# Kernel optimization log

Hardware: AMD Instinct MI355X
Metric: run time of the kernel (lower is better)

Reference implementation:

```python
import jax, jax.numpy as jnp
import numpy as np

HIDDEN = 2048
NUM_HEADS = 16
HEAD_DIM = HIDDEN // NUM_HEADS  # 128
LAYER_IDX = 0


def setup_inputs() -> dict:
    key = jax.random.key(0)
    k1, k2, k3, k4, k5 = jax.random.split(key, 5)
    B, S = 2, 2048
    hidden_states = jax.random.normal(k1, (B, S, HIDDEN), dtype=jnp.float32)
    # causal mask, broadcastable to attn shape (B, Q, H, K)
    causal = jnp.tril(jnp.ones((S, S), dtype=jnp.bool_))  # [Q, K]
    attention_mask = causal[None, :, None, :]  # [1, Q, 1, K]
    c_attn_w = jax.random.normal(k2, (HIDDEN, HIDDEN + 2 * HEAD_DIM), dtype=jnp.float32) * 0.02
    c_attn_b = jax.random.normal(k3, (HIDDEN + 2 * HEAD_DIM,), dtype=jnp.float32) * 0.02
    c_proj_w = jax.random.normal(k4, (HIDDEN, HIDDEN), dtype=jnp.float32) * 0.02
    c_proj_b = jax.random.normal(k5, (HIDDEN,), dtype=jnp.float32) * 0.02
    return {
        "hidden_states": hidden_states,
        "attention_mask": attention_mask,
        "c_attn_w": c_attn_w,
        "c_attn_b": c_attn_b,
        "c_proj_w": c_proj_w,
        "c_proj_b": c_proj_b,
    }


def reference(hidden_states, attention_mask, c_attn_w, c_attn_b, c_proj_w, c_proj_b):
    B, S, D = hidden_states.shape
    H, hd = NUM_HEADS, HEAD_DIM
    # c_attn then split into per-head query and shared (MQA) key/value
    qkv = hidden_states @ c_attn_w + c_attn_b  # [B, S, D + 2*hd]
    query = qkv[..., :D].reshape(B, S, H, hd)  # [B, Q, H, hd]
    k = qkv[..., D:D + hd]                     # [B, K, hd] shared across heads
    v = qkv[..., D + hd:]                      # [B, K, hd]
    # fp32 input => upcast=False => unscale=1, scale = 1/sqrt(head_dim)
    scale = 1.0 / jnp.sqrt(jnp.float32(hd))
    scores = jnp.einsum('bqhd,bkd->bqhk', query, k) * scale  # [B, Q, H, K]
    mask_value = jnp.finfo(jnp.float32).min
    scores = jnp.where(attention_mask, scores, mask_value)
    attn = jax.nn.softmax(scores, axis=-1)
    attn_output = jnp.einsum('bqhk,bkd->bqhd', attn, v).reshape(B, S, D)
    attn_output = attn_output @ c_proj_w + c_proj_b
    return attn_output
```

## Files before the change

### kernel.cpp

```cpp
#include <hip/hip_runtime.h>
#include <hip/hip_bf16.h>

typedef __bf16 bf16_t;
typedef __bf16 bf16x8 __attribute__((ext_vector_type(8)));
typedef __bf16 bf16x4 __attribute__((ext_vector_type(4)));
typedef float f32x4 __attribute__((ext_vector_type(4)));

#define S_LEN 2048
#define HID   2048
#define NH    16
#define HD    128
#define QKVN  2304
#define NEG_BIG (-30000.0f)

__device__ __forceinline__ void gld_lds16(const bf16_t* g, bf16_t* l) {
  __builtin_amdgcn_global_load_lds(
      (const __attribute__((address_space(1))) void*)((const void*)g),
      (__attribute__((address_space(3))) void*)((void*)l), 16, 0, 0);
}

__global__ __launch_bounds__(256) void cvt_f32_bf16_kernel(
    const float* __restrict__ in, bf16_t* __restrict__ out, int n)
{
  int i = (blockIdx.x * 256 + threadIdx.x) * 4;
  if (i < n) {
    float4 v = *(const float4*)(in + i);
    bf16x4 o;
    o[0] = (bf16_t)v.x; o[1] = (bf16_t)v.y; o[2] = (bf16_t)v.z; o[3] = (bf16_t)v.w;
    *(bf16x4*)(out + i) = o;
  }
}

__global__ __launch_bounds__(256) void transpose_cvt_kernel(
    const float* __restrict__ in, bf16_t* __restrict__ out, int K, int N)
{
  int nc = threadIdx.x & 63;
  int kg = threadIdx.x >> 6;
  int n  = blockIdx.x * 64 + nc;
  int kb = blockIdx.y * 32 + kg * 8;
  bf16x8 v;
  #pragma unroll
  for (int i = 0; i < 8; ++i) v[i] = (bf16_t)in[(size_t)(kb + i) * N + n];
  *(bf16x8*)(out + (size_t)n * K + kb) = v;
}

__global__ __launch_bounds__(256) void vt_extract_kernel(
    const bf16_t* __restrict__ qkv, bf16_t* __restrict__ vtg)
{
  int d  = threadIdx.x & 127;
  int sg = threadIdx.x >> 7;
  int b  = blockIdx.y;
  int s8 = blockIdx.x * 2 + sg;
  bf16x8 v;
  #pragma unroll
  for (int i = 0; i < 8; ++i)
    v[i] = qkv[((size_t)(b * S_LEN + s8 * 8 + i)) * QKVN + HID + HD + d];
  *(bf16x8*)(vtg + ((size_t)(b * HD + d)) * S_LEN + s8 * 8) = v;
}

template <typename OutT>
__global__ __launch_bounds__(256) void gemm_bias_kernel(
    const bf16_t* __restrict__ A, const bf16_t* __restrict__ WT,
    const float* __restrict__ bias, OutT* __restrict__ C,
    int K, int lda, int ldc)
{
  __shared__ bf16_t Ash[128 * 64];
  __shared__ bf16_t Bsh[128 * 64];

  const int tid  = threadIdx.x;
  const int wave = tid >> 6;
  const int lane = tid & 63;
  const int quad = lane >> 4;
  const int c16  = lane & 15;
  const int wm = wave >> 1;
  const int wn = wave & 1;
  const int n0 = blockIdx.x * 128;
  const int m0 = blockIdx.y * 128;

  f32x4 acc[4][4] = {};

  for (int k0 = 0; k0 < K; k0 += 64) {
    __syncthreads();
    #pragma unroll
    for (int j = 0; j < 4; ++j) {
      int cbase = wave * 256 + j * 64;
      int c = cbase + lane;
      int row = c >> 3;
      int kcl = (c ^ row) & 7;
      gld_lds16(A  + (size_t)(m0 + row) * lda + k0 + kcl * 8, Ash + cbase * 8);
      gld_lds16(WT + (size_t)(n0 + row) * K   + k0 + kcl * 8, Bsh + cbase * 8);
    }
    __syncthreads();

    #pragma unroll
    for (int kk = 0; kk < 2; ++kk) {
      bf16x8 af[4], bfr[4];
      #pragma unroll
      for (int rb = 0; rb < 4; ++rb) {
        int row = wm * 64 + rb * 16 + c16;
        int kcp = ((kk * 4 + quad) ^ row) & 7;
        af[rb] = *(const bf16x8*)(Ash + row * 64 + kcp * 8);
      }
      #pragma unroll
      for (int nt = 0; nt < 4; ++nt) {
        int row = wn * 64 + nt * 16 + c16;
        int kcp = ((kk * 4 + quad) ^ row) & 7;
        bfr[nt] = *(const bf16x8*)(Bsh + row * 64 + kcp * 8);
      }
      #pragma unroll
      for (int rb = 0; rb < 4; ++rb)
        #pragma unroll
        for (int nt = 0; nt < 4; ++nt)
          acc[rb][nt] = __builtin_amdgcn_mfma_f32_16x16x32_bf16(af[rb], bfr[nt],
                                                                acc[rb][nt], 0, 0, 0);
    }
  }

  #pragma unroll
  for (int nt = 0; nt < 4; ++nt) {
    int col = n0 + wn * 64 + nt * 16 + c16;
    float bv = bias[col];
    #pragma unroll
    for (int rb = 0; rb < 4; ++rb) {
      int rbase = m0 + wm * 64 + rb * 16 + quad * 4;
      #pragma unroll
      for (int r = 0; r < 4; ++r)
        C[(size_t)(rbase + r) * ldc + col] = (OutT)(acc[rb][nt][r] + bv);
    }
  }
}

__global__ __launch_bounds__(512, 4) void mqa_attn_kernel(
    const bf16_t* __restrict__ qkv, const bf16_t* __restrict__ vtg,
    bf16_t* __restrict__ out)
{
  __shared__ bf16_t Ksh[2][64 * 136];
  __shared__ bf16_t VTsh[2][128 * 72];

  const int tid  = threadIdx.x;
  const int wave = tid >> 6;
  const int g    = wave >> 2;
  const int wv   = wave & 3;
  const int lane = tid & 63;
  const int quad = lane >> 4;
  const int c16  = lane & 15;
  const int gt   = tid & 255;
  const int h = blockIdx.y;
  const int b = blockIdx.z;
  const float qscale = 0.08838834764831845f * 1.4426950408889634f;

  const bf16_t* kbase = qkv + (size_t)b * S_LEN * QKVN + HID;
  const bf16_t* vtb   = vtg + (size_t)b * HD * S_LEN;

  for (int half = 0; half < 2; ++half) {
    const int qb = half ? (31 - (int)blockIdx.x) : (int)blockIdx.x;
    const int q0 = qb * 64;
    const int qrow = q0 + wv * 16 + c16;

    const bf16_t* qp = qkv + ((size_t)(b * S_LEN + qrow)) * QKVN + h * HD;
    bf16x8 qf[4];
    #pragma unroll
    for (int ks = 0; ks < 4; ++ks) {
      bf16x8 t = *(const bf16x8*)(qp + ks * 32 + quad * 8);
      #pragma unroll
      for (int j = 0; j < 8; ++j) t[j] = (bf16_t)((float)t[j] * qscale);
      qf[ks] = t;
    }

    float m_q = NEG_BIG, l_q = 0.0f;
    f32x4 o[8] = {};
    const int nss = (qb + 2) >> 1;

    for (int ss = 0; ss < nss; ++ss) {
      const int kt = 2 * ss + g;
      const bool active = (kt <= qb);

      __syncthreads();
      if (active) {
        for (int c = gt; c < 1024; c += 256) {
          int key = c >> 4, dc = c & 15;
          *(bf16x8*)(&Ksh[g][key * 136 + dc * 8]) =
              *(const bf16x8*)(kbase + (size_t)(kt * 64 + key) * QKVN + dc * 8);
        }
        for (int c = gt; c < 1024; c += 256) {
          int d = c >> 3, kc = c & 7;
          *(bf16x8*)(&VTsh[g][d * 72 + kc * 8]) =
              *(const bf16x8*)(vtb + (size_t)d * S_LEN + kt * 64 + kc * 8);
        }
      }
      __syncthreads();

      float p[4][4];
      if (active) {
        f32x4 sacc[4] = {};
        #pragma unroll
        for (int mt = 0; mt < 4; ++mt) {
          #pragma unroll
          for (int ks = 0; ks < 4; ++ks) {
            bf16x8 kf = *(const bf16x8*)(&Ksh[g][(mt * 16 + c16) * 136 + ks * 32 + quad * 8]);
            sacc[mt] = __builtin_amdgcn_mfma_f32_16x16x32_bf16(kf, qf[ks], sacc[mt], 0, 0, 0);
          }
        }
        float mx = NEG_BIG;
        if (kt == qb) {
          #pragma unroll
          for (int mt = 0; mt < 4; ++mt) {
            #pragma unroll
            for (int r = 0; r < 4; ++r) {
              int key = kt * 64 + mt * 16 + quad * 4 + r;
              float v = sacc[mt][r];
              if (key > qrow) v = NEG_BIG;
              p[mt][r] = v;
              mx = fmaxf(mx, v);
            }
          }
        } else {
          #pragma unroll
          for (int mt = 0; mt < 4; ++mt) {
            #pragma unroll
            for (int r = 0; r < 4; ++r) {
              p[mt][r] = sacc[mt][r];
              mx = fmaxf(mx, sacc[mt][r]);
            }
          }
        }
        mx = fmaxf(mx, __shfl_xor(mx, 16));
        mx = fmaxf(mx, __shfl_xor(mx, 32));

        float mn = fmaxf(m_q, mx);
        float alpha = __builtin_exp2f(m_q - mn);
        m_q = mn;

        float rs = 0.f;
        #pragma unroll
        for (int mt = 0; mt < 4; ++mt) {
          #pragma unroll
          for (int r = 0; r < 4; ++r) {
            float pe = __builtin_exp2f(p[mt][r] - m_q);
            p[mt][r] = pe;
            rs += pe;
          }
        }
        rs += __shfl_xor(rs, 16);
        rs += __shfl_xor(rs, 32);
        l_q = l_q * alpha + rs;
        #pragma unroll
        for (int mt8 = 0; mt8 < 8; ++mt8) {
          #pragma unroll
          for (int r = 0; r < 4; ++r) o[mt8][r] *= alpha;
        }
      }

      __syncthreads();
      if (active) {
        bf16_t* Pw = &Ksh[g][(wv * 16) * 136];
        #pragma unroll
        for (int mt = 0; mt < 4; ++mt) {
          bf16x4 pk;
          #pragma unroll
          for (int r = 0; r < 4; ++r) pk[r] = (bf16_t)p[mt][r];
          *(bf16x4*)(Pw + c16 * 136 + mt * 16 + quad * 4) = pk;
        }
        bf16x8 pf[2];
        #pragma unroll
        for (int kh = 0; kh < 2; ++kh)
          pf[kh] = *(const bf16x8*)(Pw + c16 * 136 + kh * 32 + quad * 8);
        #pragma unroll
        for (int mt8 = 0; mt8 < 8; ++mt8) {
          #pragma unroll
          for (int kh = 0; kh < 2; ++kh) {
            bf16x8 vf = *(const bf16x8*)(&VTsh[g][(mt8 * 16 + c16) * 72 + kh * 32 + quad * 8]);
            o[mt8] = __builtin_amdgcn_mfma_f32_16x16x32_bf16(vf, pf[kh], o[mt8], 0, 0, 0);
          }
        }
      }
    }

    __syncthreads();
    float* scr = (float*)&VTsh[0][0];
    float* mls = scr + 4 * 16 * 132;
    if (g == 1) {
      float* op = scr + (wv * 16 + c16) * 132;
      #pragma unroll
      for (int mt8 = 0; mt8 < 8; ++mt8)
        *(f32x4*)(op + mt8 * 16 + quad * 4) = o[mt8];
      if (quad == 0) {
        mls[wv * 32 + c16] = m_q;
        mls[wv * 32 + 16 + c16] = l_q;
      }
    }
    __syncthreads();
    if (g == 0) {
      float m1 = mls[wv * 32 + c16];
      float l1 = mls[wv * 32 + 16 + c16];
      float mF = fmaxf(m_q, m1);
      float a0 = __builtin_exp2f(m_q - mF);
      float a1 = __builtin_exp2f(m1 - mF);
      float inv = 1.0f / fmaxf(a0 * l_q + a1 * l1, 1e-20f);
      a0 *= inv; a1 *= inv;
      const float* op = scr + (wv * 16 + c16) * 132;
      bf16_t* Osh = &Ksh[0][(wv * 16) * 136];
      #pragma unroll
      for (int mt8 = 0; mt8 < 8; ++mt8) {
        f32x4 o1 = *(const f32x4*)(op + mt8 * 16 + quad * 4);
        bf16x4 pk;
        #pragma unroll
        for (int r = 0; r < 4; ++r) pk[r] = (bf16_t)(o[mt8][r] * a0 + o1[r] * a1);
        *(bf16x4*)(Osh + c16 * 136 + mt8 * 16 + quad * 4) = pk;
      }
      int ql = lane >> 2, dc = lane & 3;
      #pragma unroll
      for (int i = 0; i < 4; ++i) {
        bf16x8 v = *(const bf16x8*)(Osh + ql * 136 + dc * 8 + i * 32);
        *(bf16x8*)(out + ((size_t)(b * S_LEN + q0 + wv * 16 + ql)) * HID
                       + h * HD + dc * 8 + i * 32) = v;
      }
    }
  }
}

extern "C" void kernel_launch(void* const* d_in, const int* in_sizes, int n_in,
                              void* d_out, int out_size, void* d_ws, size_t ws_size,
                              hipStream_t stream) {
  const float* hidden_f   = (const float*)d_in[0];
  const float* c_attn_w_f = (const float*)d_in[2];
  const float* c_attn_b_f = (const float*)d_in[3];
  const float* c_proj_w_f = (const float*)d_in[4];
  const float* c_proj_b_f = (const float*)d_in[5];
  float* out = (float*)d_out;

  const int M = 2 * S_LEN;
  const int nH  = M * HID;
  const int nWq = HID * QKVN;
  const int nWp = HID * HID;

  bf16_t* hbf   = (bf16_t*)d_ws;
  bf16_t* wqT   = hbf  + nH;
  bf16_t* wpT   = wqT  + nWq;
  bf16_t* qkv   = wpT  + nWp;
  bf16_t* attn  = qkv  + (size_t)M * QKVN;
  bf16_t* vtg   = attn + (size_t)M * HID;

  cvt_f32_bf16_kernel<<<nH / 1024, 256, 0, stream>>>(hidden_f, hbf, nH);
  dim3 gt1(QKVN / 64, HID / 32);
  transpose_cvt_kernel<<<gt1, 256, 0, stream>>>(c_attn_w_f, wqT, HID, QKVN);
  dim3 gt2(HID / 64, HID / 32);
  transpose_cvt_kernel<<<gt2, 256, 0, stream>>>(c_proj_w_f, wpT, HID, HID);

  dim3 g1(QKVN / 128, M / 128);
  gemm_bias_kernel<bf16_t><<<g1, 256, 0, stream>>>(hbf, wqT, c_attn_b_f, qkv,
                                                   HID, HID, QKVN);

  dim3 gv(S_LEN / 16, 2);
  vt_extract_kernel<<<gv, 256, 0, stream>>>(qkv, vtg);

  dim3 g2(16, NH, 2);
  mqa_attn_kernel<<<g2, 512, 0, stream>>>(qkv, vtg, attn);

  dim3 g3(HID / 128, M / 128);
  gemm_bias_kernel<float><<<g3, 256, 0, stream>>>(attn, wpT, c_proj_b_f, out,
                                                  HID, HID, HID);
}
```

Measured before the change: 341.5 us.

## Split attention waves across query blocks and narrow GEMM tiles to 128x64

The attention kernel no longer splits keys between two wave groups and merges partial softmax states at the end. Now the two groups own different query blocks (bx and 31-bx) and share one K/V tile per step, so the cross-group merge goes away and the K/V footprint drops to a single buffer, allowing higher occupancy. The GEMM tile is narrowed to 128x64 with launch bounds of 4 blocks, doubling the grid for better CU fill at the cost of more A-tile reloads. The attention loop now runs 32-bx steps for both groups, so the group with the smaller query block sits idle for part of it.

After: 519.4 us. 1.52x slower.

```diff
diff --git a/kernel.cpp b/kernel.cpp
--- a/kernel.cpp
+++ b/kernel.cpp
@@ -59,13 +59,13 @@
 }
 
 template <typename OutT>
-__global__ __launch_bounds__(256) void gemm_bias_kernel(
+__global__ __launch_bounds__(256, 4) void gemm_bias_kernel(
     const bf16_t* __restrict__ A, const bf16_t* __restrict__ WT,
     const float* __restrict__ bias, OutT* __restrict__ C,
     int K, int lda, int ldc)
 {
   __shared__ bf16_t Ash[128 * 64];
-  __shared__ bf16_t Bsh[128 * 64];
+  __shared__ bf16_t Bsh[64 * 64];
 
   const int tid  = threadIdx.x;
   const int wave = tid >> 6;
@@ -74,10 +74,10 @@
   const int c16  = lane & 15;
   const int wm = wave >> 1;
   const int wn = wave & 1;
-  const int n0 = blockIdx.x * 128;
+  const int n0 = blockIdx.x * 64;
   const int m0 = blockIdx.y * 128;
 
-  f32x4 acc[4][4] = {};
+  f32x4 acc[4][2] = {};
 
   for (int k0 = 0; k0 < K; k0 += 64) {
     __syncthreads();
@@ -87,14 +87,21 @@
       int c = cbase + lane;
       int row = c >> 3;
       int kcl = (c ^ row) & 7;
-      gld_lds16(A  + (size_t)(m0 + row) * lda + k0 + kcl * 8, Ash + cbase * 8);
-      gld_lds16(WT + (size_t)(n0 + row) * K   + k0 + kcl * 8, Bsh + cbase * 8);
+      gld_lds16(A + (size_t)(m0 + row) * lda + k0 + kcl * 8, Ash + cbase * 8);
+    }
+    #pragma unroll
+    for (int j = 0; j < 2; ++j) {
+      int cbase = wave * 128 + j * 64;
+      int c = cbase + lane;
+      int row = c >> 3;
+      int kcl = (c ^ row) & 7;
+      gld_lds16(WT + (size_t)(n0 + row) * K + k0 + kcl * 8, Bsh + cbase * 8);
     }
     __syncthreads();
 
     #pragma unroll
     for (int kk = 0; kk < 2; ++kk) {
-      bf16x8 af[4], bfr[4];
+      bf16x8 af[4], bfr[2];
       #pragma unroll
       for (int rb = 0; rb < 4; ++rb) {
         int row = wm * 64 + rb * 16 + c16;
@@ -102,23 +109,23 @@
         af[rb] = *(const bf16x8*)(Ash + row * 64 + kcp * 8);
       }
       #pragma unroll
-      for (int nt = 0; nt < 4; ++nt) {
-        int row = wn * 64 + nt * 16 + c16;
+      for (int nt = 0; nt < 2; ++nt) {
+        int row = wn * 32 + nt * 16 + c16;
         int kcp = ((kk * 4 + quad) ^ row) & 7;
         bfr[nt] = *(const bf16x8*)(Bsh + row * 64 + kcp * 8);
       }
       #pragma unroll
       for (int rb = 0; rb < 4; ++rb)
         #pragma unroll
-        for (int nt = 0; nt < 4; ++nt)
+        for (int nt = 0; nt < 2; ++nt)
           acc[rb][nt] = __builtin_amdgcn_mfma_f32_16x16x32_bf16(af[rb], bfr[nt],
                                                                 acc[rb][nt], 0, 0, 0);
     }
   }
 
   #pragma unroll
-  for (int nt = 0; nt < 4; ++nt) {
-    int col = n0 + wn * 64 + nt * 16 + c16;
+  for (int nt = 0; nt < 2; ++nt) {
+    int col = n0 + wn * 32 + nt * 16 + c16;
     float bv = bias[col];
     #pragma unroll
     for (int rb = 0; rb < 4; ++rb) {
@@ -130,12 +137,13 @@
   }
 }
 
-__global__ __launch_bounds__(512, 4) void mqa_attn_kernel(
+__global__ __launch_bounds__(512, 8) void mqa_attn_kernel(
     const bf16_t* __restrict__ qkv, const bf16_t* __restrict__ vtg,
     bf16_t* __restrict__ out)
 {
-  __shared__ bf16_t Ksh[2][64 * 136];
-  __shared__ bf16_t VTsh[2][128 * 72];
+  __shared__ bf16_t SM[64 * 136 + 128 * 72];
+  bf16_t* Ksh  = SM;
+  bf16_t* VTsh = SM + 64 * 136;
 
   const int tid  = threadIdx.x;
   const int wave = tid >> 6;
@@ -144,178 +152,150 @@
   const int lane = tid & 63;
   const int quad = lane >> 4;
   const int c16  = lane & 15;
-  const int gt   = tid & 255;
-  const int h = blockIdx.y;
-  const int b = blockIdx.z;
+  const int bx = blockIdx.x;
+  const int h  = blockIdx.y;
+  const int b  = blockIdx.z;
   const float qscale = 0.08838834764831845f * 1.4426950408889634f;
 
   const bf16_t* kbase = qkv + (size_t)b * S_LEN * QKVN + HID;
   const bf16_t* vtb   = vtg + (size_t)b * HD * S_LEN;
 
-  for (int half = 0; half < 2; ++half) {
-    const int qb = half ? (31 - (int)blockIdx.x) : (int)blockIdx.x;
-    const int q0 = qb * 64;
-    const int qrow = q0 + wv * 16 + c16;
-
-    const bf16_t* qp = qkv + ((size_t)(b * S_LEN + qrow)) * QKVN + h * HD;
-    bf16x8 qf[4];
-    #pragma unroll
-    for (int ks = 0; ks < 4; ++ks) {
-      bf16x8 t = *(const bf16x8*)(qp + ks * 32 + quad * 8);
-      #pragma unroll
-      for (int j = 0; j < 8; ++j) t[j] = (bf16_t)((float)t[j] * qscale);
-      qf[ks] = t;
-    }
-
-    float m_q = NEG_BIG, l_q = 0.0f;
-    f32x4 o[8] = {};
-    const int nss = (qb + 2) >> 1;
-
-    for (int ss = 0; ss < nss; ++ss) {
-      const int kt = 2 * ss + g;
-      const bool active = (kt <= qb);
-
-      __syncthreads();
-      if (active) {
-        for (int c = gt; c < 1024; c += 256) {
-          int key = c >> 4, dc = c & 15;
-          *(bf16x8*)(&Ksh[g][key * 136 + dc * 8]) =
-              *(const bf16x8*)(kbase + (size_t)(kt * 64 + key) * QKVN + dc * 8);
-        }
-        for (int c = gt; c < 1024; c += 256) {
-          int d = c >> 3, kc = c & 7;
-          *(bf16x8*)(&VTsh[g][d * 72 + kc * 8]) =
-              *(const bf16x8*)(vtb + (size_t)d * S_LEN + kt * 64 + kc * 8);
-        }
-      }
-      __syncthreads();
-
-      float p[4][4];
-      if (active) {
-        f32x4 sacc[4] = {};
-        #pragma unroll
-        for (int mt = 0; mt < 4; ++mt) {
-          #pragma unroll
-          for (int ks = 0; ks < 4; ++ks) {
-            bf16x8 kf = *(const bf16x8*)(&Ksh[g][(mt * 16 + c16) * 136 + ks * 32 + quad * 8]);
-            sacc[mt] = __builtin_amdgcn_mfma_f32_16x16x32_bf16(kf, qf[ks], sacc[mt], 0, 0, 0);
-          }
-        }
-        float mx = NEG_BIG;
-        if (kt == qb) {
-          #pragma unroll
-          for (int mt = 0; mt < 4; ++mt) {
-            #pragma unroll
-            for (int r = 0; r < 4; ++r) {
-              int key = kt * 64 + mt * 16 + quad * 4 + r;
-              float v = sacc[mt][r];
-              if (key > qrow) v = NEG_BIG;
-              p[mt][r] = v;
-              mx = fmaxf(mx, v);
-            }
-          }
-        } else {
-          #pragma unroll
-          for (int mt = 0; mt < 4; ++mt) {
-            #pragma unroll
-            for (int r = 0; r < 4; ++r) {
-              p[mt][r] = sacc[mt][r];
-              mx = fmaxf(mx, sacc[mt][r]);
-            }
-          }
-        }
-        mx = fmaxf(mx, __shfl_xor(mx, 16));
-        mx = fmaxf(mx, __shfl_xor(mx, 32));
-
-        float mn = fmaxf(m_q, mx);
-        float alpha = __builtin_exp2f(m_q - mn);
-        m_q = mn;
-
-        float rs = 0.f;
+  const int qb = g ? (31 - bx) : bx;
+  const int q0 = qb * 64;
+  const int qrow = q0 + wv * 16 + c16;
+
+  const bf16_t* qp = qkv + ((size_t)(b * S_LEN + qrow)) * QKVN + h * HD;
+  bf16x8 qf[4];
+  #pragma unroll
+  for (int ks = 0; ks < 4; ++ks) {
+    bf16x8 t = *(const bf16x8*)(qp + ks * 32 + quad * 8);
+    #pragma unroll
+    for (int j = 0; j < 8; ++j) t[j] = (bf16_t)((float)t[j] * qscale);
+    qf[ks] = t;
+  }
+
+  float m_q = NEG_BIG, l_q = 0.0f;
+  f32x4 o[8] = {};
+  const int nss = 32 - bx;
+
+  for (int kt = 0; kt < nss; ++kt) {
+    const bool active = (kt <= qb);
+
+    __syncthreads();
+    for (int c = tid; c < 1024; c += 512) {
+      int key = c >> 4, dc = c & 15;
+      *(bf16x8*)(Ksh + key * 136 + dc * 8) =
+          *(const bf16x8*)(kbase + (size_t)(kt * 64 + key) * QKVN + dc * 8);
+    }
+    for (int c = tid; c < 1024; c += 512) {
+      int d = c >> 3, kc = c & 7;
+      *(bf16x8*)(VTsh + d * 72 + kc * 8) =
+          *(const bf16x8*)(vtb + (size_t)d * S_LEN + kt * 64 + kc * 8);
+    }
+    __syncthreads();
+
+    float p[4][4];
+    if (active) {
+      f32x4 sacc[4] = {};
+      #pragma unroll
+      for (int mt = 0; mt < 4; ++mt) {
+        #pragma unroll
+        for (int ks = 0; ks < 4; ++ks) {
+          bf16x8 kf = *(const bf16x8*)(Ksh + (mt * 16 + c16) * 136 + ks * 32 + quad * 8);
+          sacc[mt] = __builtin_amdgcn_mfma_f32_16x16x32_bf16(kf, qf[ks], sacc[mt], 0, 0, 0);
+        }
+      }
+      float mx = NEG_BIG;
+      if (kt == qb) {
         #pragma unroll
         for (int mt = 0; mt < 4; ++mt) {
           #pragma unroll
           for (int r = 0; r < 4; ++r) {
-            float pe = __builtin_exp2f(p[mt][r] - m_q);
-            p[mt][r] = pe;
-            rs += pe;
+            int key = kt * 64 + mt * 16 + quad * 4 + r;
+            float v = sacc[mt][r];
+            if (key > qrow) v = NEG_BIG;
+            p[mt][r] = v;
+            mx = fmaxf(mx, v);
           }
         }
-        rs += __shfl_xor(rs, 16);
-        rs += __shfl_xor(rs, 32);
-        l_q = l_q * alpha + rs;
-        #pragma unroll
-        for (int mt8 = 0; mt8 < 8; ++mt8) {
+      } else {
+        #pragma unroll
+        for (int mt = 0; mt < 4; ++mt) {
           #pragma unroll
-          for (int r = 0; r < 4; ++r) o[mt8][r] *= alpha;
-        }
-      }
-
-      __syncthreads();
-      if (active) {
-        bf16_t* Pw = &Ksh[g][(wv * 16) * 136];
-        #pragma unroll
-        for (int mt = 0; mt < 4; ++mt) {
-          bf16x4 pk;
-          #pragma unroll
-          for (int r = 0; r < 4; ++r) pk[r] = (bf16_t)p[mt][r];
-          *(bf16x4*)(Pw + c16 * 136 + mt * 16 + quad * 4) = pk;
-        }
-        bf16x8 pf[2];
-        #pragma unroll
-        for (int kh = 0; kh < 2; ++kh)
-          pf[kh] = *(const bf16x8*)(Pw + c16 * 136 + kh * 32 + quad * 8);
-        #pragma unroll
-        for (int mt8 = 0; mt8 < 8; ++mt8) {
-          #pragma unroll
-          for (int kh = 0; kh < 2; ++kh) {
-            bf16x8 vf = *(const bf16x8*)(&VTsh[g][(mt8 * 16 + c16) * 72 + kh * 32 + quad * 8]);
-            o[mt8] = __builtin_amdgcn_mfma_f32_16x16x32_bf16(vf, pf[kh], o[mt8], 0, 0, 0);
+          for (int r = 0; r < 4; ++r) {
+            p[mt][r] = sacc[mt][r];
+            mx = fmaxf(mx, sacc[mt][r]);
           }
         }
       }
-    }
-
-    __syncthreads();
-    float* scr = (float*)&VTsh[0][0];
-    float* mls = scr + 4 * 16 * 132;
-    if (g == 1) {
-      float* op = scr + (wv * 16 + c16) * 132;
-      #pragma unroll
-      for (int mt8 = 0; mt8 < 8; ++mt8)
-        *(f32x4*)(op + mt8 * 16 + quad * 4) = o[mt8];
-      if (quad == 0) {
-        mls[wv * 32 + c16] = m_q;
-        mls[wv * 32 + 16 + c16] = l_q;
-      }
-    }
-    __syncthreads();
-    if (g == 0) {
-      float m1 = mls[wv * 32 + c16];
-      float l1 = mls[wv * 32 + 16 + c16];
-      float mF = fmaxf(m_q, m1);
-      float a0 = __builtin_exp2f(m_q - mF);
-      float a1 = __builtin_exp2f(m1 - mF);
-      float inv = 1.0f / fmaxf(a0 * l_q + a1 * l1, 1e-20f);
-      a0 *= inv; a1 *= inv;
-      const float* op = scr + (wv * 16 + c16) * 132;
-      bf16_t* Osh = &Ksh[0][(wv * 16) * 136];
+      mx = fmaxf(mx, __shfl_xor(mx, 16));
+      mx = fmaxf(mx, __shfl_xor(mx, 32));
+
+      float mn = fmaxf(m_q, mx);
+      float alpha = __builtin_exp2f(m_q - mn);
+      m_q = mn;
+
+      float rs = 0.f;
+      #pragma unroll
+      for (int mt = 0; mt < 4; ++mt) {
+        #pragma unroll
+        for (int r = 0; r < 4; ++r) {
+          float pe = __builtin_exp2f(p[mt][r] - m_q);
+          p[mt][r] = pe;
+          rs += pe;
+        }
+      }
+      rs += __shfl_xor(rs, 16);
+      rs += __shfl_xor(rs, 32);
+      l_q = l_q * alpha + rs;
       #pragma unroll
       for (int mt8 = 0; mt8 < 8; ++mt8) {
-        f32x4 o1 = *(const f32x4*)(op + mt8 * 16 + quad * 4);
+        #pragma unroll
+        for (int r = 0; r < 4; ++r) o[mt8][r] *= alpha;
+      }
+    }
+
+    __syncthreads();
+    if (active) {
+      bf16_t* Pw = Ksh + (wv * 16) * 136 + g * 72;
+      #pragma unroll
+      for (int mt = 0; mt < 4; ++mt) {
         bf16x4 pk;
         #pragma unroll
-        for (int r = 0; r < 4; ++r) pk[r] = (bf16_t)(o[mt8][r] * a0 + o1[r] * a1);
-        *(bf16x4*)(Osh + c16 * 136 + mt8 * 16 + quad * 4) = pk;
-      }
-      int ql = lane >> 2, dc = lane & 3;
-      #pragma unroll
-      for (int i = 0; i < 4; ++i) {
-        bf16x8 v = *(const bf16x8*)(Osh + ql * 136 + dc * 8 + i * 32);
-        *(bf16x8*)(out + ((size_t)(b * S_LEN + q0 + wv * 16 + ql)) * HID
-                       + h * HD + dc * 8 + i * 32) = v;
-      }
-    }
+        for (int r = 0; r < 4; ++r) pk[r] = (bf16_t)p[mt][r];
+        *(bf16x4*)(Pw + c16 * 136 + mt * 16 + quad * 4) = pk;
+      }
+      bf16x8 pf[2];
+      #pragma unroll
+      for (int kh = 0; kh < 2; ++kh)
+        pf[kh] = *(const bf16x8*)(Pw + c16 * 136 + kh * 32 + quad * 8);
+      #pragma unroll
+      for (int mt8 = 0; mt8 < 8; ++mt8) {
+        #pragma unroll
+        for (int kh = 0; kh < 2; ++kh) {
+          bf16x8 vf = *(const bf16x8*)(VTsh + (mt8 * 16 + c16) * 72 + kh * 32 + quad * 8);
+          o[mt8] = __builtin_amdgcn_mfma_f32_16x16x32_bf16(vf, pf[kh], o[mt8], 0, 0, 0);
+        }
+      }
+    }
+  }
+
+  __syncthreads();
+  float inv = 1.0f / fmaxf(l_q, 1e-20f);
+  bf16_t* Osh = SM + wave * (16 * 136);
+  #pragma unroll
+  for (int mt8 = 0; mt8 < 8; ++mt8) {
+    bf16x4 pk;
+    #pragma unroll
+    for (int r = 0; r < 4; ++r) pk[r] = (bf16_t)(o[mt8][r] * inv);
+    *(bf16x4*)(Osh + c16 * 136 + mt8 * 16 + quad * 4) = pk;
+  }
+  int ql = lane >> 2, dc = lane & 3;
+  #pragma unroll
+  for (int i = 0; i < 4; ++i) {
+    bf16x8 v = *(const bf16x8*)(Osh + ql * 136 + dc * 8 + i * 32);
+    *(bf16x8*)(out + ((size_t)(b * S_LEN + q0 + wv * 16 + ql)) * HID
+                   + h * HD + dc * 8 + i * 32) = v;
   }
 }
 
@@ -347,7 +327,7 @@
   dim3 gt2(HID / 64, HID / 32);
   transpose_cvt_kernel<<<gt2, 256, 0, stream>>>(c_proj_w_f, wpT, HID, HID);
 
-  dim3 g1(QKVN / 128, M / 128);
+  dim3 g1(QKVN / 64, M / 128);
   gemm_bias_kernel<bf16_t><<<g1, 256, 0, stream>>>(hbf, wqT, c_attn_b_f, qkv,
                                                    HID, HID, QKVN);
 
@@ -357,7 +337,7 @@
   dim3 g2(16, NH, 2);
   mqa_attn_kernel<<<g2, 512, 0, stream>>>(qkv, vtg, attn);
 
-  dim3 g3(HID / 128, M / 128);
+  dim3 g3(HID / 64, M / 128);
   gemm_bias_kernel<float><<<g3, 256, 0, stream>>>(attn, wpT, c_proj_b_f, out,
                                                   HID, HID, HID);
 }
```
